# Kernel tuning notes

Measured on AMD Instinct MI355X. Metric: run time of the kernel, lower is better.

Reference implementation:

```python
import jax, jax.numpy as jnp
import numpy as np

N_NODES = 100000
N_EDGES = 1600000
IN_CH = 128
HEADS = 4
OUT_CH = 32
NEG_SLOPE = 0.2
DIV_WEIGHT = 0.1
EPS_SOFTMAX = 1e-16  # PyG softmax eps
EPS_COS = 1e-8       # F.cosine_similarity eps


def setup_inputs() -> dict:
    key = jax.random.key(0)
    k1, k2, k3, k4, k5 = jax.random.split(key, 5)
    x = jax.random.normal(k1, (N_NODES, IN_CH), dtype=jnp.float32)
    # edge_index with guaranteed no self loops (remove_self_loops becomes a no-op)
    row = jax.random.randint(k2, (N_EDGES,), 0, N_NODES, dtype=jnp.int32)
    off = jax.random.randint(k3, (N_EDGES,), 1, N_NODES, dtype=jnp.int32)
    col = (row + off) % N_NODES
    edge_index = jnp.stack([row, col], axis=0)
    # params (xavier-ish scale)
    W = jax.random.normal(k4, (HEADS * OUT_CH, IN_CH), dtype=jnp.float32) * np.sqrt(2.0 / (IN_CH + HEADS * OUT_CH))
    att = jax.random.normal(k5, (1, HEADS, 2 * OUT_CH), dtype=jnp.float32) * np.sqrt(2.0 / (1 + 2 * OUT_CH))
    bias = jnp.zeros((HEADS * OUT_CH,), dtype=jnp.float32)
    return {"x": x, "edge_index": edge_index, "W": W, "att": att, "bias": bias}


def reference(x, edge_index, W, att, bias):
    N = x.shape[0]
    H = att.shape[1]
    C = att.shape[2] // 2
    idx_dtype = edge_index.dtype
    # add self loops (input has none, so remove_self_loops is a no-op)
    loops = jnp.arange(N, dtype=idx_dtype)
    row = jnp.concatenate([edge_index[0], loops])  # destination
    col = jnp.concatenate([edge_index[1], loops])  # source
    # linear projection -> [N, H, C]
    h = (x @ W.T).reshape(N, H, C)
    # attention logits: (cat(x_i, x_j) * att).sum(-1) == s_i[row] + s_j[col]
    s_i = jnp.einsum('nhc,hc->nh', h, att[0, :, :C])  # [N, H]
    s_j = jnp.einsum('nhc,hc->nh', h, att[0, :, C:])  # [N, H]
    e = s_i[row] + s_j[col]                            # [E, H]
    e = jnp.where(e >= 0, e, NEG_SLOPE * e)            # leaky_relu
    # segment softmax over destination node (row)
    e_max = jax.ops.segment_max(e, row, num_segments=N)
    e_max = jnp.where(jnp.isfinite(e_max), e_max, 0.0)
    e_exp = jnp.exp(e - e_max[row])
    denom = jax.ops.segment_sum(e_exp, row, num_segments=N)
    alpha = e_exp / (denom[row] + EPS_SOFTMAX)         # [E, H]
    # attention diversity loss: mean pairwise cosine sim (zero diagonal)
    gram = alpha.T @ alpha                             # [H, H]
    norms = jnp.sqrt(jnp.diag(gram))
    corr = gram / jnp.maximum(norms[:, None] * norms[None, :], EPS_COS)
    corr = corr * (1.0 - jnp.eye(H, dtype=corr.dtype))
    diversity_loss = jnp.mean(corr) * DIV_WEIGHT
    # weighted message + scatter-add aggregation (dropout p=0 -> identity)
    msg = h[col] * alpha[:, :, None]                   # [E, H, C]
    out = jax.ops.segment_sum(msg, row, num_segments=N)
    out = out.reshape(N, H * C) + bias                 # concat=True
    return out, diversity_loss
```

## Files before the change

### kernel.cpp

```cpp
#include <hip/hip_runtime.h>
#include <math.h>

#define HC     128
#define SLOT   64
#define AGG_BLOCKS 2048
#define PREP_GRID  2048
#define NPART  8

typedef unsigned int uint32;
typedef unsigned long long uint64;
typedef short bf16x8 __attribute__((ext_vector_type(8)));
typedef float f32x4 __attribute__((ext_vector_type(4)));

__device__ inline unsigned short f2bf(float f){
  uint32 u = __float_as_uint(f);
  u = (u + 0x7fffu + ((u >> 16) & 1u)) >> 16;
  return (unsigned short)u;
}
__device__ inline uint32 pack_bf2(float a, float b){
  return (uint32)f2bf(a) | ((uint32)f2bf(b) << 16);
}
__device__ inline void lds_fence(){
  asm volatile("s_waitcnt lgkmcnt(0)" ::: "memory");
  __builtin_amdgcn_sched_barrier(0);
}


__global__ __launch_bounds__(256) void k_init(const float* __restrict__ W, unsigned short* __restrict__ W_bf,
                                              int* cnt, int N){
  int gid = blockIdx.x*256 + threadIdx.x;
  if (gid < 8192){
    float2 v = *(const float2*)&W[2*gid];
    *(uint32*)&W_bf[2*gid] = pack_bf2(v.x, v.y);
  }
  for (int i = gid; i < N; i += gridDim.x*256) cnt[i] = 0;
}


__global__ __launch_bounds__(256) void k_prep(const float* __restrict__ x, const unsigned short* __restrict__ W_bf,
                                              const float* __restrict__ att,
                                              const int* __restrict__ row, const int* __restrict__ col,
                                              int* cnt, int* bucket,
                                              uint32* __restrict__ h_pair,
                                              float* __restrict__ s_i, float* __restrict__ s_j,
                                              int N, int E, int ntiles){
  int t = threadIdx.x;
  bool hasTile = ((int)blockIdx.x < ntiles);

  if (hasTile){
    int w = t >> 6, l = t & 63;
    int o = l & 15, lg = l >> 4;
    int n0 = blockIdx.x * 64;

    int arow = n0 + w*16 + o;
    bool rok = (arow < N);
    const float* xr = x + (size_t)arow*128;
    bf16x8 afr[4];
    #pragma unroll
    for (int ks = 0; ks < 4; ++ks){
      f32x4 a0 = (f32x4){0.f,0.f,0.f,0.f}, a1 = a0;
      if (rok){
        a0 = __builtin_nontemporal_load((const f32x4*)&xr[ks*32 + lg*8]);
        a1 = __builtin_nontemporal_load((const f32x4*)&xr[ks*32 + lg*8 + 4]);
      }
      bf16x8 pa;
      pa[0]=(short)f2bf(a0[0]); pa[1]=(short)f2bf(a0[1]); pa[2]=(short)f2bf(a0[2]); pa[3]=(short)f2bf(a0[3]);
      pa[4]=(short)f2bf(a1[0]); pa[5]=(short)f2bf(a1[1]); pa[6]=(short)f2bf(a1[2]); pa[7]=(short)f2bf(a1[3]);
      afr[ks] = pa;
    }

    f32x4 acc[8];
    #pragma unroll
    for (int cf = 0; cf < 8; ++cf) acc[cf] = (f32x4){0.f,0.f,0.f,0.f};

    #pragma unroll
    for (int ks = 0; ks < 4; ++ks){
      #pragma unroll
      for (int cf = 0; cf < 8; ++cf){
        int rb = cf*16 + o;
        bf16x8 bfr = *(const bf16x8*)&W_bf[(size_t)rb*128 + ks*32 + lg*8];
        acc[cf] = __builtin_amdgcn_mfma_f32_16x16x32_bf16(afr[ks], bfr, acc[cf], 0, 0, 0);
      }
    }

    float ai0[4], ai1[4], aj0[4], aj1[4];
    #pragma unroll
    for (int hd = 0; hd < 4; ++hd){
      ai0[hd] = att[hd*64 + o];
      ai1[hd] = att[hd*64 + 16 + o];
      aj0[hd] = att[hd*64 + 32 + o];
      aj1[hd] = att[hd*64 + 48 + o];
    }

    #pragma unroll
    for (int q = 0; q < 4; ++q){
      int node = n0 + w*16 + lg*4 + q;
      float v[8];
      #pragma unroll
      for (int cf = 0; cf < 8; ++cf) v[cf] = acc[cf][q];
      float pi[4], pj[4];
      #pragma unroll
      for (int hd = 0; hd < 4; ++hd){
        pi[hd] = v[2*hd]*ai0[hd] + v[2*hd+1]*ai1[hd];
        pj[hd] = v[2*hd]*aj0[hd] + v[2*hd+1]*aj1[hd];
      }
      #pragma unroll
      for (int sh = 1; sh < 16; sh <<= 1){
        #pragma unroll
        for (int hd = 0; hd < 4; ++hd){
          pi[hd] += __shfl_xor(pi[hd], sh);
          pj[hd] += __shfl_xor(pj[hd], sh);
        }
      }
      if (node < N){
        #pragma unroll
        for (int hd = 0; hd < 4; ++hd)
          __builtin_nontemporal_store(pack_bf2(v[2*hd], v[2*hd+1]),
                                      &h_pair[(size_t)node*64 + hd*16 + o]);
        if (o == 0){
          f32x4 vi = (f32x4){pi[0], pi[1], pi[2], pi[3]};
          f32x4 vj = (f32x4){pj[0], pj[1], pj[2], pj[3]};
          __builtin_nontemporal_store(vi, (f32x4*)&s_i[(size_t)node*4]);
          __builtin_nontemporal_store(vj, (f32x4*)&s_j[(size_t)node*4]);
        }
      }
    }
  }

  {
    int k = blockIdx.x & (NPART-1);
    int c = blockIdx.x >> 3;
    int CH = PREP_GRID / NPART;
    int per  = (E + CH - 1) / CH;
    int base = c * per;
    int end  = base + per; if (end > E) end = E;
    int rng  = (N + NPART - 1) / NPART;
    int lo = k * rng, hi = lo + rng;
    for (int i = base + t; i < end; i += 256){
      int d = row[i];
      if (d >= lo && d < hi){
        int pos = atomicAdd(&cnt[d], 1);
        if (pos < SLOT-1) bucket[(size_t)d*SLOT + pos] = col[i];
      }
    }
  }
}


__global__ __launch_bounds__(256) void k_agg(const uint32* __restrict__ h_pair, const float* __restrict__ s_i,
                                             const float* __restrict__ s_j, const int* __restrict__ cnt,
                                             const int* __restrict__ bucket,
                                             const float* __restrict__ bias, float* __restrict__ out,
                                             float* __restrict__ gram_part, int N){
  __shared__ __align__(16) float al[4][SLOT*4];
  __shared__ int   cs[4][SLOT];
  __shared__ float red[4][10];
  const uint2* hp2 = (const uint2*)h_pair;
  int t = threadIdx.x;
  int w = t >> 6, l = t & 63;
  int g = l >> 4, o = l & 15;
  int lw = l & 31, half = l >> 5;
  int g2 = lw >> 3;
  int o0 = (2*lw) & 15;
  int cbase = 32*g2 + (half << 4) + o0;
  float2 bv = *(const float2*)&bias[cbase];
  float ga[10];
  #pragma unroll
  for (int p = 0; p < 10; ++p) ga[p] = 0.f;
  int TW = gridDim.x * 4;

  for (int n = blockIdx.x*4 + w; n < N; n += TW){
    int dc = cnt[n]; if (dc > SLOT-1) dc = SLOT-1;
    int d  = dc + 1;
    float4 si = *(const float4*)&s_i[(size_t)n*4];
    if (l < d){
      int src = (l < dc) ? __builtin_nontemporal_load(&bucket[(size_t)n*SLOT + l]) : n;
      cs[w][l] = src << 5;
      float4 sj = *(const float4*)&s_j[(size_t)src*4];
      float4 e;
      e.x = si.x + sj.x; e.y = si.y + sj.y; e.z = si.z + sj.z; e.w = si.w + sj.w;
      e.x = e.x >= 0.f ? e.x : 0.2f*e.x;
      e.y = e.y >= 0.f ? e.y : 0.2f*e.y;
      e.z = e.z >= 0.f ? e.z : 0.2f*e.z;
      e.w = e.w >= 0.f ? e.w : 0.2f*e.w;
      *(float4*)&al[w][l*4] = e;
    }
    if ((d & 1) && l == d){
      cs[w][l] = n << 5;
      *(float4*)&al[w][l*4] = make_float4(0.f,0.f,0.f,0.f);
    }
    lds_fence();
    float m = -3.4e38f;
    for (int j = o; j < d; j += 16) m = fmaxf(m, al[w][j*4 + g]);
    #pragma unroll
    for (int sh = 1; sh < 16; sh <<= 1) m = fmaxf(m, __shfl_xor(m, sh));
    float sum = 0.f;
    for (int j = o; j < d; j += 16){
      float v = __expf(al[w][j*4 + g] - m);
      al[w][j*4 + g] = v;
      sum += v;
    }
    #pragma unroll
    for (int sh = 1; sh < 16; sh <<= 1) sum += __shfl_xor(sum, sh);
    float r = 1.f/(sum + 1e-16f);
    for (int j = o; j < d; j += 16) al[w][j*4 + g] *= r;
    lds_fence();
    if (l < d){
      float4 a = *(const float4*)&al[w][l*4];
      ga[0] += a.x*a.x; ga[1] += a.x*a.y; ga[2] += a.x*a.z; ga[3] += a.x*a.w;
      ga[4] += a.y*a.y; ga[5] += a.y*a.z; ga[6] += a.y*a.w;
      ga[7] += a.z*a.z; ga[8] += a.z*a.w;
      ga[9] += a.w*a.w;
    }
    float a0 = 0.f, a1 = 0.f, a2 = 0.f, a3 = 0.f;
    const float* alw = &al[w][0];
    const int*   csw = &cs[w][0];
    int npair = (d + 1) >> 1;
    int i = 0;
    for (; i + 4 <= npair; i += 4){
      int e0 = 2*i + half, e1 = e0 + 2, e2 = e0 + 4, e3 = e0 + 6;
      int s0 = csw[e0], s1 = csw[e1], s2 = csw[e2], s3 = csw[e3];
      float w0 = alw[e0*4 + g2], w1 = alw[e1*4 + g2];
      float w2 = alw[e2*4 + g2], w3 = alw[e3*4 + g2];
      uint2 v0 = hp2[(size_t)(uint32)(s0 + lw)];
      uint2 v1 = hp2[(size_t)(uint32)(s1 + lw)];
      uint2 v2 = hp2[(size_t)(uint32)(s2 + lw)];
      uint2 v3 = hp2[(size_t)(uint32)(s3 + lw)];
      a0 += w0 * __uint_as_float(v0.x << 16);  a1 += w0 * __uint_as_float(v0.x & 0xffff0000u);
      a2 += w0 * __uint_as_float(v0.y << 16);  a3 += w0 * __uint_as_float(v0.y & 0xffff0000u);
      a0 += w1 * __uint_as_float(v1.x << 16);  a1 += w1 * __uint_as_float(v1.x & 0xffff0000u);
      a2 += w1 * __uint_as_float(v1.y << 16);  a3 += w1 * __uint_as_float(v1.y & 0xffff0000u);
      a0 += w2 * __uint_as_float(v2.x << 16);  a1 += w2 * __uint_as_float(v2.x & 0xffff0000u);
      a2 += w2 * __uint_as_float(v2.y << 16);  a3 += w2 * __uint_as_float(v2.y & 0xffff0000u);
      a0 += w3 * __uint_as_float(v3.x << 16);  a1 += w3 * __uint_as_float(v3.x & 0xffff0000u);
      a2 += w3 * __uint_as_float(v3.y << 16);  a3 += w3 * __uint_as_float(v3.y & 0xffff0000u);
    }
    for (; i < npair; ++i){
      int e = 2*i + half;
      float aw = alw[e*4 + g2];
      uint2 v = hp2[(size_t)(uint32)(csw[e] + lw)];
      a0 += aw * __uint_as_float(v.x << 16);  a1 += aw * __uint_as_float(v.x & 0xffff0000u);
      a2 += aw * __uint_as_float(v.y << 16);  a3 += aw * __uint_as_float(v.y & 0xffff0000u);
    }
    a0 += __shfl_xor(a0, 32);
    a1 += __shfl_xor(a1, 32);
    a2 += __shfl_xor(a2, 32);
    a3 += __shfl_xor(a3, 32);
    union { float f[2]; uint64 u; } st;
    st.f[0] = (half ? a1 : a0) + bv.x;
    st.f[1] = (half ? a3 : a2) + bv.y;
    __builtin_nontemporal_store(st.u, (uint64*)&out[(size_t)n*128 + cbase]);
    lds_fence();
  }
  __syncthreads();
  #pragma unroll
  for (int p = 0; p < 10; ++p){
    float v = ga[p];
    #pragma unroll
    for (int sh = 1; sh < 64; sh <<= 1) v += __shfl_xor(v, sh);
    ga[p] = v;
  }
  if (l == 0){
    #pragma unroll
    for (int p = 0; p < 10; ++p) red[w][p] = ga[p];
  }
  __syncthreads();
  if (t == 0){
    #pragma unroll
    for (int p = 0; p < 10; ++p)
      gram_part[(size_t)blockIdx.x*10 + p] = red[0][p] + red[1][p] + red[2][p] + red[3][p];
  }
}


__global__ __launch_bounds__(256) void k_final(const float* __restrict__ gram_part, int nparts,
                                               float* __restrict__ loss){
  __shared__ float red[4][10];
  int t = threadIdx.x;
  float acc[10];
  #pragma unroll
  for (int p = 0; p < 10; ++p) acc[p] = 0.f;
  for (int i = t; i < nparts; i += 256){
    #pragma unroll
    for (int p = 0; p < 10; ++p) acc[p] += gram_part[(size_t)i*10 + p];
  }
  #pragma unroll
  for (int p = 0; p < 10; ++p){
    float v = acc[p];
    #pragma unroll
    for (int sh = 1; sh < 64; sh <<= 1) v += __shfl_xor(v, sh);
    acc[p] = v;
  }
  if ((t & 63) == 0){
    #pragma unroll
    for (int p = 0; p < 10; ++p) red[t >> 6][p] = acc[p];
  }
  __syncthreads();
  if (t == 0){
    float gs[10];
    #pragma unroll
    for (int p = 0; p < 10; ++p) gs[p] = red[0][p] + red[1][p] + red[2][p] + red[3][p];
    float G[4][4];
    G[0][0]=gs[0]; G[0][1]=gs[1]; G[0][2]=gs[2]; G[0][3]=gs[3];
    G[1][0]=gs[1]; G[1][1]=gs[4]; G[1][2]=gs[5]; G[1][3]=gs[6];
    G[2][0]=gs[2]; G[2][1]=gs[5]; G[2][2]=gs[7]; G[2][3]=gs[8];
    G[3][0]=gs[3]; G[3][1]=gs[6]; G[3][2]=gs[8]; G[3][3]=gs[9];
    float nr[4];
    for (int i = 0; i < 4; ++i) nr[i] = sqrtf(G[i][i]);
    float ssum = 0.f;
    for (int i = 0; i < 4; ++i)
      for (int j = 0; j < 4; ++j)
        if (i != j) ssum += G[i][j] / fmaxf(nr[i]*nr[j], 1e-8f);
    loss[0] = ssum * (0.1f/16.f);
  }
}


extern "C" void kernel_launch(void* const* d_in, const int* in_sizes, int n_in,
                              void* d_out, int out_size, void* d_ws, size_t ws_size,
                              hipStream_t stream){
  const float* x    = (const float*)d_in[0];
  const int*   edge = (const int*)d_in[1];
  const float* W    = (const float*)d_in[2];
  const float* att  = (const float*)d_in[3];
  const float* bias = (const float*)d_in[4];
  int N = in_sizes[0] / 128;
  int E = in_sizes[1] / 2;
  const int* row = edge;
  const int* col = edge + E;
  float* out  = (float*)d_out;
  float* loss = out + (size_t)N*HC;

  char* wsb = (char*)d_ws;
  size_t off = 0;
  auto alloc = [&](size_t bytes)->void*{
    size_t o = (off + 255) & ~(size_t)255;
    off = o + bytes;
    return (void*)(wsb + o);
  };
  uint32* h_pair   = (uint32*)alloc((size_t)N*64*sizeof(uint32));
  float* s_i       = (float*)alloc((size_t)N*4*sizeof(float));
  float* s_j       = (float*)alloc((size_t)N*4*sizeof(float));
  int*   cnt       = (int*)alloc((size_t)N*sizeof(int));
  int*   bucket    = (int*)alloc((size_t)N*SLOT*sizeof(int));
  unsigned short* W_bf = (unsigned short*)alloc(16384*sizeof(unsigned short));
  float* gram_part = (float*)alloc((size_t)AGG_BLOCKS*10*sizeof(float));
  (void)ws_size; (void)n_in; (void)out_size;

  k_init<<<128,256,0,stream>>>(W, W_bf, cnt, N);
  int ntiles = (N+63)/64;
  k_prep<<<PREP_GRID,256,0,stream>>>(x, W_bf, att, row, col, cnt, bucket, h_pair, s_i, s_j, N, E, ntiles);
  k_agg<<<AGG_BLOCKS,256,0,stream>>>(h_pair, s_i, s_j, cnt, bucket, bias, out, gram_part, N);
  k_final<<<1,256,0,stream>>>(gram_part, AGG_BLOCKS, loss);
}
```

Baseline: 228.9 us.

## Replace per-node atomic bucketing with two-pass coarse partition and LDS scatter

The old single pass, fused with the GEMM, had every block rescan its slice of the edge list once per node-range filter, doing global atomics per destination node. The new version first partitions edges into 256-node coarse buckets with one global atomic per edge, packing the local destination and source into one word. A second kernel then uses LDS atomics per bucket to build the per-node adjacency lists and counts. The GEMM moves into its own kernel, which adds launches and a staging buffer and drops the overlap between GEMM and bucketing. The fixed per-bucket capacity CAP could overflow on skewed inputs, and the 17-bit source packing limits N to 131072.

Measured after the change: 735.0 us. 221% more time.

```diff
diff --git a/kernel.cpp b/kernel.cpp
--- a/kernel.cpp
+++ b/kernel.cpp
@@ -4,13 +4,14 @@
 #define HC     128
 #define SLOT   64
 #define AGG_BLOCKS 2048
-#define PREP_GRID  2048
-#define NPART  8
+#define CAP    4608
+#define BSH    8
 
 typedef unsigned int uint32;
 typedef unsigned long long uint64;
 typedef short bf16x8 __attribute__((ext_vector_type(8)));
 typedef float f32x4 __attribute__((ext_vector_type(4)));
+typedef int   i32x4 __attribute__((ext_vector_type(4)));
 
 __device__ inline unsigned short f2bf(float f){
   uint32 u = __float_as_uint(f);
@@ -27,120 +28,142 @@
 
 
 __global__ __launch_bounds__(256) void k_init(const float* __restrict__ W, unsigned short* __restrict__ W_bf,
-                                              int* cnt, int N){
+                                              int* pcnt, int NB){
   int gid = blockIdx.x*256 + threadIdx.x;
   if (gid < 8192){
     float2 v = *(const float2*)&W[2*gid];
     *(uint32*)&W_bf[2*gid] = pack_bf2(v.x, v.y);
   }
-  for (int i = gid; i < N; i += gridDim.x*256) cnt[i] = 0;
-}
-
-
-__global__ __launch_bounds__(256) void k_prep(const float* __restrict__ x, const unsigned short* __restrict__ W_bf,
+  if (gid < NB) pcnt[gid] = 0;
+}
+
+
+__global__ __launch_bounds__(256) void k_part(const int* __restrict__ row, const int* __restrict__ col,
+                                              int* pcnt, uint32* __restrict__ pbuf, int E){
+  int gid = blockIdx.x*256 + threadIdx.x;
+  int i = gid*4;
+  if (i + 4 <= E){
+    i32x4 r4 = __builtin_nontemporal_load((const i32x4*)&row[i]);
+    i32x4 c4 = __builtin_nontemporal_load((const i32x4*)&col[i]);
+    #pragma unroll
+    for (int q = 0; q < 4; ++q){
+      int d = r4[q], s = c4[q];
+      int b = d >> BSH;
+      int pos = atomicAdd(&pcnt[b], 1);
+      if (pos < CAP) pbuf[(size_t)b*CAP + pos] = ((uint32)(d & 255) << 17) | (uint32)s;
+    }
+  } else {
+    for (; i < E; ++i){
+      int d = row[i], s = col[i];
+      int b = d >> BSH;
+      int pos = atomicAdd(&pcnt[b], 1);
+      if (pos < CAP) pbuf[(size_t)b*CAP + pos] = ((uint32)(d & 255) << 17) | (uint32)s;
+    }
+  }
+}
+
+
+__global__ __launch_bounds__(256) void k_scatter(const int* __restrict__ pcnt, const uint32* __restrict__ pbuf,
+                                                 int* __restrict__ cnt, int* __restrict__ bucket, int N){
+  __shared__ int lcnt[256];
+  int t = threadIdx.x;
+  int b = blockIdx.x;
+  lcnt[t] = 0;
+  __syncthreads();
+  int ne = pcnt[b]; if (ne > CAP) ne = CAP;
+  int dbase = b << BSH;
+  for (int i = t; i < ne; i += 256){
+    uint32 e = __builtin_nontemporal_load(&pbuf[(size_t)b*CAP + i]);
+    int s  = (int)(e & 0x1FFFFu);
+    int dl = (int)(e >> 17);
+    int pos = atomicAdd(&lcnt[dl], 1);
+    if (pos < SLOT-1) bucket[(size_t)(dbase + dl)*SLOT + pos] = s;
+  }
+  __syncthreads();
+  int d = dbase + t;
+  if (d < N) cnt[d] = lcnt[t];
+}
+
+
+__global__ __launch_bounds__(256) void k_gemm(const float* __restrict__ x, const unsigned short* __restrict__ W_bf,
                                               const float* __restrict__ att,
-                                              const int* __restrict__ row, const int* __restrict__ col,
-                                              int* cnt, int* bucket,
                                               uint32* __restrict__ h_pair,
-                                              float* __restrict__ s_i, float* __restrict__ s_j,
-                                              int N, int E, int ntiles){
+                                              float* __restrict__ s_i, float* __restrict__ s_j, int N){
   int t = threadIdx.x;
-  bool hasTile = ((int)blockIdx.x < ntiles);
-
-  if (hasTile){
-    int w = t >> 6, l = t & 63;
-    int o = l & 15, lg = l >> 4;
-    int n0 = blockIdx.x * 64;
-
-    int arow = n0 + w*16 + o;
-    bool rok = (arow < N);
-    const float* xr = x + (size_t)arow*128;
-    bf16x8 afr[4];
-    #pragma unroll
-    for (int ks = 0; ks < 4; ++ks){
-      f32x4 a0 = (f32x4){0.f,0.f,0.f,0.f}, a1 = a0;
-      if (rok){
-        a0 = __builtin_nontemporal_load((const f32x4*)&xr[ks*32 + lg*8]);
-        a1 = __builtin_nontemporal_load((const f32x4*)&xr[ks*32 + lg*8 + 4]);
-      }
-      bf16x8 pa;
-      pa[0]=(short)f2bf(a0[0]); pa[1]=(short)f2bf(a0[1]); pa[2]=(short)f2bf(a0[2]); pa[3]=(short)f2bf(a0[3]);
-      pa[4]=(short)f2bf(a1[0]); pa[5]=(short)f2bf(a1[1]); pa[6]=(short)f2bf(a1[2]); pa[7]=(short)f2bf(a1[3]);
-      afr[ks] = pa;
-    }
-
-    f32x4 acc[8];
-    #pragma unroll
-    for (int cf = 0; cf < 8; ++cf) acc[cf] = (f32x4){0.f,0.f,0.f,0.f};
-
-    #pragma unroll
-    for (int ks = 0; ks < 4; ++ks){
-      #pragma unroll
-      for (int cf = 0; cf < 8; ++cf){
-        int rb = cf*16 + o;
-        bf16x8 bfr = *(const bf16x8*)&W_bf[(size_t)rb*128 + ks*32 + lg*8];
-        acc[cf] = __builtin_amdgcn_mfma_f32_16x16x32_bf16(afr[ks], bfr, acc[cf], 0, 0, 0);
-      }
-    }
-
-    float ai0[4], ai1[4], aj0[4], aj1[4];
+  int w = t >> 6, l = t & 63;
+  int o = l & 15, lg = l >> 4;
+  int n0 = blockIdx.x * 64;
+
+  int arow = n0 + w*16 + o;
+  bool rok = (arow < N);
+  const float* xr = x + (size_t)arow*128;
+  bf16x8 afr[4];
+  #pragma unroll
+  for (int ks = 0; ks < 4; ++ks){
+    f32x4 a0 = (f32x4){0.f,0.f,0.f,0.f}, a1 = a0;
+    if (rok){
+      a0 = __builtin_nontemporal_load((const f32x4*)&xr[ks*32 + lg*8]);
+      a1 = __builtin_nontemporal_load((const f32x4*)&xr[ks*32 + lg*8 + 4]);
+    }
+    bf16x8 pa;
+    pa[0]=(short)f2bf(a0[0]); pa[1]=(short)f2bf(a0[1]); pa[2]=(short)f2bf(a0[2]); pa[3]=(short)f2bf(a0[3]);
+    pa[4]=(short)f2bf(a1[0]); pa[5]=(short)f2bf(a1[1]); pa[6]=(short)f2bf(a1[2]); pa[7]=(short)f2bf(a1[3]);
+    afr[ks] = pa;
+  }
+
+  f32x4 acc[8];
+  #pragma unroll
+  for (int cf = 0; cf < 8; ++cf) acc[cf] = (f32x4){0.f,0.f,0.f,0.f};
+
+  #pragma unroll
+  for (int ks = 0; ks < 4; ++ks){
+    #pragma unroll
+    for (int cf = 0; cf < 8; ++cf){
+      int rb = cf*16 + o;
+      bf16x8 bfr = *(const bf16x8*)&W_bf[(size_t)rb*128 + ks*32 + lg*8];
+      acc[cf] = __builtin_amdgcn_mfma_f32_16x16x32_bf16(afr[ks], bfr, acc[cf], 0, 0, 0);
+    }
+  }
+
+  float ai0[4], ai1[4], aj0[4], aj1[4];
+  #pragma unroll
+  for (int hd = 0; hd < 4; ++hd){
+    ai0[hd] = att[hd*64 + o];
+    ai1[hd] = att[hd*64 + 16 + o];
+    aj0[hd] = att[hd*64 + 32 + o];
+    aj1[hd] = att[hd*64 + 48 + o];
+  }
+
+  #pragma unroll
+  for (int q = 0; q < 4; ++q){
+    int node = n0 + w*16 + lg*4 + q;
+    float v[8];
+    #pragma unroll
+    for (int cf = 0; cf < 8; ++cf) v[cf] = acc[cf][q];
+    float pi[4], pj[4];
     #pragma unroll
     for (int hd = 0; hd < 4; ++hd){
-      ai0[hd] = att[hd*64 + o];
-      ai1[hd] = att[hd*64 + 16 + o];
-      aj0[hd] = att[hd*64 + 32 + o];
-      aj1[hd] = att[hd*64 + 48 + o];
-    }
-
-    #pragma unroll
-    for (int q = 0; q < 4; ++q){
-      int node = n0 + w*16 + lg*4 + q;
-      float v[8];
-      #pragma unroll
-      for (int cf = 0; cf < 8; ++cf) v[cf] = acc[cf][q];
-      float pi[4], pj[4];
+      pi[hd] = v[2*hd]*ai0[hd] + v[2*hd+1]*ai1[hd];
+      pj[hd] = v[2*hd]*aj0[hd] + v[2*hd+1]*aj1[hd];
+    }
+    #pragma unroll
+    for (int sh = 1; sh < 16; sh <<= 1){
       #pragma unroll
       for (int hd = 0; hd < 4; ++hd){
-        pi[hd] = v[2*hd]*ai0[hd] + v[2*hd+1]*ai1[hd];
-        pj[hd] = v[2*hd]*aj0[hd] + v[2*hd+1]*aj1[hd];
+        pi[hd] += __shfl_xor(pi[hd], sh);
+        pj[hd] += __shfl_xor(pj[hd], sh);
       }
+    }
+    if (node < N){
       #pragma unroll
-      for (int sh = 1; sh < 16; sh <<= 1){
-        #pragma unroll
-        for (int hd = 0; hd < 4; ++hd){
-          pi[hd] += __shfl_xor(pi[hd], sh);
-          pj[hd] += __shfl_xor(pj[hd], sh);
-        }
-      }
-      if (node < N){
-        #pragma unroll
-        for (int hd = 0; hd < 4; ++hd)
-          __builtin_nontemporal_store(pack_bf2(v[2*hd], v[2*hd+1]),
-                                      &h_pair[(size_t)node*64 + hd*16 + o]);
-        if (o == 0){
-          f32x4 vi = (f32x4){pi[0], pi[1], pi[2], pi[3]};
-          f32x4 vj = (f32x4){pj[0], pj[1], pj[2], pj[3]};
-          __builtin_nontemporal_store(vi, (f32x4*)&s_i[(size_t)node*4]);
-          __builtin_nontemporal_store(vj, (f32x4*)&s_j[(size_t)node*4]);
-        }
-      }
-    }
-  }
-
-  {
-    int k = blockIdx.x & (NPART-1);
-    int c = blockIdx.x >> 3;
-    int CH = PREP_GRID / NPART;
-    int per  = (E + CH - 1) / CH;
-    int base = c * per;
-    int end  = base + per; if (end > E) end = E;
-    int rng  = (N + NPART - 1) / NPART;
-    int lo = k * rng, hi = lo + rng;
-    for (int i = base + t; i < end; i += 256){
-      int d = row[i];
-      if (d >= lo && d < hi){
-        int pos = atomicAdd(&cnt[d], 1);
-        if (pos < SLOT-1) bucket[(size_t)d*SLOT + pos] = col[i];
+      for (int hd = 0; hd < 4; ++hd)
+        __builtin_nontemporal_store(pack_bf2(v[2*hd], v[2*hd+1]),
+                                    &h_pair[(size_t)node*64 + hd*16 + o]);
+      if (o == 0){
+        f32x4 vi = (f32x4){pi[0], pi[1], pi[2], pi[3]};
+        f32x4 vj = (f32x4){pj[0], pj[1], pj[2], pj[3]};
+        __builtin_nontemporal_store(vi, (f32x4*)&s_i[(size_t)node*4]);
+        __builtin_nontemporal_store(vj, (f32x4*)&s_j[(size_t)node*4]);
       }
     }
   }
@@ -331,6 +354,8 @@
   float* out  = (float*)d_out;
   float* loss = out + (size_t)N*HC;
 
+  int NB = (N + 255) >> BSH;
+
   char* wsb = (char*)d_ws;
   size_t off = 0;
   auto alloc = [&](size_t bytes)->void*{
@@ -343,13 +368,18 @@
   float* s_j       = (float*)alloc((size_t)N*4*sizeof(float));
   int*   cnt       = (int*)alloc((size_t)N*sizeof(int));
   int*   bucket    = (int*)alloc((size_t)N*SLOT*sizeof(int));
+  int*   pcnt      = (int*)alloc((size_t)NB*sizeof(int));
+  uint32* pbuf     = (uint32*)alloc((size_t)NB*CAP*sizeof(uint32));
   unsigned short* W_bf = (unsigned short*)alloc(16384*sizeof(unsigned short));
   float* gram_part = (float*)alloc((size_t)AGG_BLOCKS*10*sizeof(float));
   (void)ws_size; (void)n_in; (void)out_size;
 
-  k_init<<<128,256,0,stream>>>(W, W_bf, cnt, N);
-  int ntiles = (N+63)/64;
-  k_prep<<<PREP_GRID,256,0,stream>>>(x, W_bf, att, row, col, cnt, bucket, h_pair, s_i, s_j, N, E, ntiles);
+  k_init<<<64,256,0,stream>>>(W, W_bf, pcnt, NB);
+  int PB = (E + 4*256 - 1) / (4*256);
+  k_part<<<PB,256,0,stream>>>(row, col, pcnt, pbuf, E);
+  k_scatter<<<NB,256,0,stream>>>(pcnt, pbuf, cnt, bucket, N);
+  int GB = (N+63)/64;
+  k_gemm<<<GB,256,0,stream>>>(x, W_bf, att, h_pair, s_i, s_j, N);
   k_agg<<<AGG_BLOCKS,256,0,stream>>>(h_pair, s_i, s_j, cnt, bucket, bias, out, gram_part, N);
   k_final<<<1,256,0,stream>>>(gram_part, AGG_BLOCKS, loss);
 }
```

## Split fused prep kernel into separate bucket-fill and GEMM kernels

Applied to the files above, without the earlier changes.

Splits the combined projection-plus-bucketing kernel into two launches: k_fill, which builds per-destination edge buckets with atomics, and k_gemm, which runs the MFMA projection and attention scores. The fill kernel now reads row and col as 4-wide vector nontemporal loads, using 256 chunks times 8 node partitions. This is meant to stop the GEMM tiles and the atomic scatter from competing for resources inside the same block, and to cut edge-load instruction count. The cost is an extra kernel launch, and the two phases no longer overlap within one kernel.

New measurement: 238.3 us. +4.1%, slower.

```diff
diff --git a/kernel.cpp b/kernel.cpp
--- a/kernel.cpp
+++ b/kernel.cpp
@@ -4,13 +4,14 @@
 #define HC     128
 #define SLOT   64
 #define AGG_BLOCKS 2048
-#define PREP_GRID  2048
 #define NPART  8
+#define CHUNKS 256
 
 typedef unsigned int uint32;
 typedef unsigned long long uint64;
 typedef short bf16x8 __attribute__((ext_vector_type(8)));
 typedef float f32x4 __attribute__((ext_vector_type(4)));
+typedef int   i32x4 __attribute__((ext_vector_type(4)));
 
 __device__ inline unsigned short f2bf(float f){
   uint32 u = __float_as_uint(f);
@@ -37,110 +38,120 @@
 }
 
 
-__global__ __launch_bounds__(256) void k_prep(const float* __restrict__ x, const unsigned short* __restrict__ W_bf,
+__global__ __launch_bounds__(256) void k_fill(const int* __restrict__ row, const int* __restrict__ col,
+                                              int* cnt, int* bucket, int E, int N){
+  int k = blockIdx.x & (NPART-1);
+  int c = blockIdx.x >> 3;
+  int per  = (((E + CHUNKS - 1) / CHUNKS) + 3) & ~3;
+  int base = c * per;
+  int end  = base + per; if (end > E) end = E;
+  int rng  = (N + NPART - 1) / NPART;
+  int lo = k * rng, hi = lo + rng;
+  int t = threadIdx.x;
+  for (int i = base + t*4; i < end; i += 256*4){
+    if (i + 4 <= end){
+      i32x4 r4 = __builtin_nontemporal_load((const i32x4*)&row[i]);
+      i32x4 c4 = __builtin_nontemporal_load((const i32x4*)&col[i]);
+      #pragma unroll
+      for (int q = 0; q < 4; ++q){
+        int d = r4[q];
+        if (d >= lo && d < hi){
+          int pos = atomicAdd(&cnt[d], 1);
+          if (pos < SLOT-1) bucket[(size_t)d*SLOT + pos] = c4[q];
+        }
+      }
+    } else {
+      for (int j = i; j < end; ++j){
+        int d = row[j];
+        if (d >= lo && d < hi){
+          int pos = atomicAdd(&cnt[d], 1);
+          if (pos < SLOT-1) bucket[(size_t)d*SLOT + pos] = col[j];
+        }
+      }
+    }
+  }
+}
+
+
+__global__ __launch_bounds__(256) void k_gemm(const float* __restrict__ x, const unsigned short* __restrict__ W_bf,
                                               const float* __restrict__ att,
-                                              const int* __restrict__ row, const int* __restrict__ col,
-                                              int* cnt, int* bucket,
                                               uint32* __restrict__ h_pair,
-                                              float* __restrict__ s_i, float* __restrict__ s_j,
-                                              int N, int E, int ntiles){
+                                              float* __restrict__ s_i, float* __restrict__ s_j, int N){
   int t = threadIdx.x;
-  bool hasTile = ((int)blockIdx.x < ntiles);
-
-  if (hasTile){
-    int w = t >> 6, l = t & 63;
-    int o = l & 15, lg = l >> 4;
-    int n0 = blockIdx.x * 64;
-
-    int arow = n0 + w*16 + o;
-    bool rok = (arow < N);
-    const float* xr = x + (size_t)arow*128;
-    bf16x8 afr[4];
-    #pragma unroll
-    for (int ks = 0; ks < 4; ++ks){
-      f32x4 a0 = (f32x4){0.f,0.f,0.f,0.f}, a1 = a0;
-      if (rok){
-        a0 = __builtin_nontemporal_load((const f32x4*)&xr[ks*32 + lg*8]);
-        a1 = __builtin_nontemporal_load((const f32x4*)&xr[ks*32 + lg*8 + 4]);
-      }
-      bf16x8 pa;
-      pa[0]=(short)f2bf(a0[0]); pa[1]=(short)f2bf(a0[1]); pa[2]=(short)f2bf(a0[2]); pa[3]=(short)f2bf(a0[3]);
-      pa[4]=(short)f2bf(a1[0]); pa[5]=(short)f2bf(a1[1]); pa[6]=(short)f2bf(a1[2]); pa[7]=(short)f2bf(a1[3]);
-      afr[ks] = pa;
-    }
-
-    f32x4 acc[8];
-    #pragma unroll
-    for (int cf = 0; cf < 8; ++cf) acc[cf] = (f32x4){0.f,0.f,0.f,0.f};
-
-    #pragma unroll
-    for (int ks = 0; ks < 4; ++ks){
-      #pragma unroll
-      for (int cf = 0; cf < 8; ++cf){
-        int rb = cf*16 + o;
-        bf16x8 bfr = *(const bf16x8*)&W_bf[(size_t)rb*128 + ks*32 + lg*8];
-        acc[cf] = __builtin_amdgcn_mfma_f32_16x16x32_bf16(afr[ks], bfr, acc[cf], 0, 0, 0);
-      }
-    }
-
-    float ai0[4], ai1[4], aj0[4], aj1[4];
+  int w = t >> 6, l = t & 63;
+  int o = l & 15, lg = l >> 4;
+  int n0 = blockIdx.x * 64;
+
+  int arow = n0 + w*16 + o;
+  bool rok = (arow < N);
+  const float* xr = x + (size_t)arow*128;
+  bf16x8 afr[4];
+  #pragma unroll
+  for (int ks = 0; ks < 4; ++ks){
+    f32x4 a0 = (f32x4){0.f,0.f,0.f,0.f}, a1 = a0;
+    if (rok){
+      a0 = __builtin_nontemporal_load((const f32x4*)&xr[ks*32 + lg*8]);
+      a1 = __builtin_nontemporal_load((const f32x4*)&xr[ks*32 + lg*8 + 4]);
+    }
+    bf16x8 pa;
+    pa[0]=(short)f2bf(a0[0]); pa[1]=(short)f2bf(a0[1]); pa[2]=(short)f2bf(a0[2]); pa[3]=(short)f2bf(a0[3]);
+    pa[4]=(short)f2bf(a1[0]); pa[5]=(short)f2bf(a1[1]); pa[6]=(short)f2bf(a1[2]); pa[7]=(short)f2bf(a1[3]);
+    afr[ks] = pa;
+  }
+
+  f32x4 acc[8];
+  #pragma unroll
+  for (int cf = 0; cf < 8; ++cf) acc[cf] = (f32x4){0.f,0.f,0.f,0.f};
+
+  #pragma unroll
+  for (int ks = 0; ks < 4; ++ks){
+    #pragma unroll
+    for (int cf = 0; cf < 8; ++cf){
+      int rb = cf*16 + o;
+      bf16x8 bfr = *(const bf16x8*)&W_bf[(size_t)rb*128 + ks*32 + lg*8];
+      acc[cf] = __builtin_amdgcn_mfma_f32_16x16x32_bf16(afr[ks], bfr, acc[cf], 0, 0, 0);
+    }
+  }
+
+  float ai0[4], ai1[4], aj0[4], aj1[4];
+  #pragma unroll
+  for (int hd = 0; hd < 4; ++hd){
+    ai0[hd] = att[hd*64 + o];
+    ai1[hd] = att[hd*64 + 16 + o];
+    aj0[hd] = att[hd*64 + 32 + o];
+    aj1[hd] = att[hd*64 + 48 + o];
+  }
+
+  #pragma unroll
+  for (int q = 0; q < 4; ++q){
+    int node = n0 + w*16 + lg*4 + q;
+    float v[8];
+    #pragma unroll
+    for (int cf = 0; cf < 8; ++cf) v[cf] = acc[cf][q];
+    float pi[4], pj[4];
     #pragma unroll
     for (int hd = 0; hd < 4; ++hd){
-      ai0[hd] = att[hd*64 + o];
-      ai1[hd] = att[hd*64 + 16 + o];
-      aj0[hd] = att[hd*64 + 32 + o];
-      aj1[hd] = att[hd*64 + 48 + o];
-    }
-
-    #pragma unroll
-    for (int q = 0; q < 4; ++q){
-      int node = n0 + w*16 + lg*4 + q;
-      float v[8];
-      #pragma unroll
-      for (int cf = 0; cf < 8; ++cf) v[cf] = acc[cf][q];
-      float pi[4], pj[4];
+      pi[hd] = v[2*hd]*ai0[hd] + v[2*hd+1]*ai1[hd];
+      pj[hd] = v[2*hd]*aj0[hd] + v[2*hd+1]*aj1[hd];
+    }
+    #pragma unroll
+    for (int sh = 1; sh < 16; sh <<= 1){
       #pragma unroll
       for (int hd = 0; hd < 4; ++hd){
-        pi[hd] = v[2*hd]*ai0[hd] + v[2*hd+1]*ai1[hd];
-        pj[hd] = v[2*hd]*aj0[hd] + v[2*hd+1]*aj1[hd];
+        pi[hd] += __shfl_xor(pi[hd], sh);
+        pj[hd] += __shfl_xor(pj[hd], sh);
       }
+    }
+    if (node < N){
       #pragma unroll
-      for (int sh = 1; sh < 16; sh <<= 1){
-        #pragma unroll
-        for (int hd = 0; hd < 4; ++hd){
-          pi[hd] += __shfl_xor(pi[hd], sh);
-          pj[hd] += __shfl_xor(pj[hd], sh);
-        }
-      }
-      if (node < N){
-        #pragma unroll
-        for (int hd = 0; hd < 4; ++hd)
-          __builtin_nontemporal_store(pack_bf2(v[2*hd], v[2*hd+1]),
-                                      &h_pair[(size_t)node*64 + hd*16 + o]);
-        if (o == 0){
-          f32x4 vi = (f32x4){pi[0], pi[1], pi[2], pi[3]};
-          f32x4 vj = (f32x4){pj[0], pj[1], pj[2], pj[3]};
-          __builtin_nontemporal_store(vi, (f32x4*)&s_i[(size_t)node*4]);
-          __builtin_nontemporal_store(vj, (f32x4*)&s_j[(size_t)node*4]);
-        }
-      }
-    }
-  }
-
-  {
-    int k = blockIdx.x & (NPART-1);
-    int c = blockIdx.x >> 3;
-    int CH = PREP_GRID / NPART;
-    int per  = (E + CH - 1) / CH;
-    int base = c * per;
-    int end  = base + per; if (end > E) end = E;
-    int rng  = (N + NPART - 1) / NPART;
-    int lo = k * rng, hi = lo + rng;
-    for (int i = base + t; i < end; i += 256){
-      int d = row[i];
-      if (d >= lo && d < hi){
-        int pos = atomicAdd(&cnt[d], 1);
-        if (pos < SLOT-1) bucket[(size_t)d*SLOT + pos] = col[i];
+      for (int hd = 0; hd < 4; ++hd)
+        __builtin_nontemporal_store(pack_bf2(v[2*hd], v[2*hd+1]),
+                                    &h_pair[(size_t)node*64 + hd*16 + o]);
+      if (o == 0){
+        f32x4 vi = (f32x4){pi[0], pi[1], pi[2], pi[3]};
+        f32x4 vj = (f32x4){pj[0], pj[1], pj[2], pj[3]};
+        __builtin_nontemporal_store(vi, (f32x4*)&s_i[(size_t)node*4]);
+        __builtin_nontemporal_store(vj, (f32x4*)&s_j[(size_t)node*4]);
       }
     }
   }
@@ -348,8 +359,9 @@
   (void)ws_size; (void)n_in; (void)out_size;
 
   k_init<<<128,256,0,stream>>>(W, W_bf, cnt, N);
-  int ntiles = (N+63)/64;
-  k_prep<<<PREP_GRID,256,0,stream>>>(x, W_bf, att, row, col, cnt, bucket, h_pair, s_i, s_j, N, E, ntiles);
+  k_fill<<<CHUNKS*NPART,256,0,stream>>>(row, col, cnt, bucket, E, N);
+  int GB = (N+63)/64;
+  k_gemm<<<GB,256,0,stream>>>(x, W_bf, att, h_pair, s_i, s_j, N);
   k_agg<<<AGG_BLOCKS,256,0,stream>>>(h_pair, s_i, s_j, cnt, bucket, bias, out, gram_part, N);
   k_final<<<1,256,0,stream>>>(gram_part, AGG_BLOCKS, loss);
 }
```
